# Kernel tuning notes

Hardware: AMD Instinct MI355X
Metric: run time of the kernel (lower is better)

Reference implementation:

```python
import jax, jax.numpy as jnp
import numpy as np

N_HEADS = 16
D_EMBD = 1024
D_HEAD = D_EMBD // N_HEADS
NEG_INF = -jnp.inf


def setup_inputs() -> dict:
    key = jax.random.key(0)
    k1, k2, k3, k4, k5 = jax.random.split(key, 5)
    b, s = 4, 2048
    scale_in = 1.0 / np.sqrt(D_EMBD)
    return {
        "x": jax.random.normal(k1, (b, s, D_EMBD), dtype=jnp.float32),
        "W_in": jax.random.normal(k2, (D_EMBD, 3 * D_EMBD), dtype=jnp.float32) * scale_in,
        "b_in": jax.random.normal(k3, (3 * D_EMBD,), dtype=jnp.float32) * 0.01,
        "W_out": jax.random.normal(k4, (D_EMBD, D_EMBD), dtype=jnp.float32) * scale_in,
        "b_out": jax.random.normal(k5, (D_EMBD,), dtype=jnp.float32) * 0.01,
    }


def reference(x, W_in, b_in, W_out, b_out):
    b, s, d = x.shape
    qkv = x @ W_in + b_in                      # [b, s, 3d]
    q, k, v = jnp.split(qkv, 3, axis=-1)
    # [b, s, d] -> [b, h, s, dh]
    def heads(t):
        return t.reshape(b, s, N_HEADS, D_HEAD).transpose(0, 2, 1, 3)
    q, k, v = heads(q), heads(k), heads(v)
    scores = jnp.einsum("bhqd,bhkd->bhqk", q, k)  # [b, h, s, s]
    # causal mask: mask strictly-upper triangle (future positions) with -inf,
    # applied before the sqrt(d_head) scale as in the original (equivalent math)
    mask = jnp.triu(jnp.ones((s, s), dtype=bool), k=1)
    scores = jnp.where(mask, NEG_INF, scores)
    scores = scores / jnp.sqrt(jnp.float32(D_HEAD)).astype(scores.dtype)
    attn = jax.nn.softmax(scores, axis=-1)
    out = jnp.einsum("bhqk,bhkd->bhqd", attn, v)   # [b, h, s, dh]
    out = out.transpose(0, 2, 1, 3).reshape(b, s, d)
    return out @ W_out + b_out
```

## Files before the change

### kernel.cpp

```cpp
#include <hip/hip_runtime.h>
#include <stdint.h>

#define AS1 __attribute__((address_space(1)))
#define AS3 __attribute__((address_space(3)))

typedef __bf16 bf16x8 __attribute__((ext_vector_type(8)));
typedef float f32x4 __attribute__((ext_vector_type(4)));
typedef unsigned short u16;
typedef unsigned int u32;

#define LOG2E 1.4426950408889634f

__device__ __forceinline__ u16 f2b(float f) {
    u32 u = __builtin_bit_cast(u32, f);
    u = (u + 0x7fffu + ((u >> 16) & 1u)) >> 16;
    return (u16)u;
}

__device__ __forceinline__ void gld16(const u16* g, u16* l) {
    __builtin_amdgcn_global_load_lds((const AS1 void*)g, (AS3 void*)l, 16, 0, 0);
}

__global__ void k_cvt(const float* __restrict__ in, u16* __restrict__ out, int n4) {
    int i = blockIdx.x * 256 + threadIdx.x;
    if (i >= n4) return;
    float4 v = reinterpret_cast<const float4*>(in)[i];
    ushort4 o;
    o.x = f2b(v.x); o.y = f2b(v.y); o.z = f2b(v.z); o.w = f2b(v.w);
    reinterpret_cast<ushort4*>(out)[i] = o;
}

__global__ void k_tr(const float* __restrict__ in, u16* __restrict__ out, int R, int C) {
    __shared__ float tl[64][65];
    int c0 = blockIdx.x * 64, r0 = blockIdx.y * 64;
    int tx = threadIdx.x & 63, ty = threadIdx.x >> 6;
#pragma unroll
    for (int i = 0; i < 16; ++i) {
        int r = i * 4 + ty;
        tl[r][tx] = in[(size_t)(r0 + r) * C + c0 + tx];
    }
    __syncthreads();
#pragma unroll
    for (int i = 0; i < 16; ++i) {
        int c = i * 4 + ty;
        out[(size_t)(c0 + c) * R + r0 + tx] = f2b(tl[tx][c]);
    }
}

template <int EPI>
__global__ __launch_bounds__(256, 2)
void k_gemm(const u16* __restrict__ A, const u16* __restrict__ BT,
            const float* __restrict__ bias,
            u16* __restrict__ qk, u16* __restrict__ vT,
            float* __restrict__ outf, int M, int N, int K) {
    __shared__ u16 sA[128 * 64];
    __shared__ u16 sB[128 * 64];
    const int t = threadIdx.x;
    const int lane = t & 63;
    const int w = t >> 6;
    const int lo = lane & 15, hi = lane >> 4;
    const int wr = w >> 1, wc = w & 1;
    const int m0 = blockIdx.x * 128, n0 = blockIdx.y * 128;

    const int srow = lane >> 3;
    const int scol = ((lane & 7) ^ srow) * 8;
    const int chunk0 = w * 4;

    f32x4 acc[4][4];
#pragma unroll
    for (int i = 0; i < 4; ++i)
#pragma unroll
        for (int j = 0; j < 4; ++j) acc[i][j] = f32x4{0.f, 0.f, 0.f, 0.f};

    char* sAc = (char*)sA;
    char* sBc = (char*)sB;

    for (int kt = 0; kt < K; kt += 64) {
        const u16* Ab = A + (size_t)m0 * K + kt;
        const u16* Bb = BT + (size_t)n0 * K + kt;
#pragma unroll
        for (int c = 0; c < 4; ++c) {
            int chunk = chunk0 + c;
            int row = chunk * 8 + srow;
            gld16(Ab + (size_t)row * K + scol, (u16*)(sAc + chunk * 1024));
            gld16(Bb + (size_t)row * K + scol, (u16*)(sBc + chunk * 1024));
        }
        __syncthreads();
#pragma unroll
        for (int ks = 0; ks < 2; ++ks) {
            bf16x8 af[4], bfr[4];
#pragma unroll
            for (int mf = 0; mf < 4; ++mf) {
                int row = wr * 64 + mf * 16 + lo;
                int byte = row * 128 + (((ks * 32 + hi * 8) * 2) ^ ((row & 7) << 4));
                af[mf] = *(const bf16x8*)(sAc + byte);
            }
#pragma unroll
            for (int nf = 0; nf < 4; ++nf) {
                int row = wc * 64 + nf * 16 + lo;
                int byte = row * 128 + (((ks * 32 + hi * 8) * 2) ^ ((row & 7) << 4));
                bfr[nf] = *(const bf16x8*)(sBc + byte);
            }
#pragma unroll
            for (int mf = 0; mf < 4; ++mf)
#pragma unroll
                for (int nf = 0; nf < 4; ++nf)
                    acc[mf][nf] = __builtin_amdgcn_mfma_f32_16x16x32_bf16(
                        af[mf], bfr[nf], acc[mf][nf], 0, 0, 0);
        }
        __syncthreads();
    }

    if (EPI == 0) {
#pragma unroll
        for (int nf = 0; nf < 4; ++nf) {
            int col = n0 + wc * 64 + nf * 16 + lo;
            float bv = bias[col];
#pragma unroll
            for (int mf = 0; mf < 4; ++mf) {
                int rowb = m0 + wr * 64 + mf * 16 + hi * 4;
                if (col < 2048) {
#pragma unroll
                    for (int r = 0; r < 4; ++r)
                        qk[(size_t)(rowb + r) * 2048 + col] = f2b(acc[mf][nf][r] + bv);
                } else {
                    int hd = col - 2048;
                    int hh = hd >> 6, dh = hd & 63;
                    int bb = rowb >> 11, s = rowb & 2047;
                    size_t base = ((size_t)(bb * 16 + hh) * 64 + dh) * 2048 + s;
#pragma unroll
                    for (int r = 0; r < 4; ++r)
                        vT[base + r] = f2b(acc[mf][nf][r] + bv);
                }
            }
        }
    } else {
#pragma unroll
        for (int nf = 0; nf < 4; ++nf) {
            int col = n0 + wc * 64 + nf * 16 + lo;
            float bv = bias[col];
#pragma unroll
            for (int mf = 0; mf < 4; ++mf) {
                int rowb = m0 + wr * 64 + mf * 16 + hi * 4;
#pragma unroll
                for (int r = 0; r < 4; ++r)
                    outf[(size_t)(rowb + r) * (size_t)N + col] = acc[mf][nf][r] + bv;
            }
        }
    }
}

__global__ __launch_bounds__(64, 4)
void k_attn(const u16* __restrict__ qk, const u16* __restrict__ vT,
            u16* __restrict__ attnout) {
    __shared__ u16 p_lds[16 * 128];
    const int lane = threadIdx.x & 63;
    const int lo = lane & 15, hi = lane >> 4;
    const int orig = blockIdx.x;
    const int wgid = (orig & 7) * 512 + (orig >> 3);
    const int j0 = wgid & 63;
    const int bh = wgid >> 6;
    const int h = bh & 15, b = bh >> 4;
    const int bS = b * 2048;
    const u16* vb = vT + (size_t)bh * (64 * 2048);
    const u16* kb = qk + (size_t)bS * 2048 + 1024 + h * 64;
    char* pb = (char*)p_lds;
    const float C1 = 0.125f * LOG2E;
    const int rsw = (lo & 7) << 4;

#pragma unroll 1
    for (int task = 0; task < 2; ++task) {
        const int j = task ? (127 - j0) : j0;
        const int qr0 = j * 16;
        const int qtile = j >> 3;
        const int qrow = qr0 + lo;

        bf16x8 qf[2];
#pragma unroll
        for (int ks = 0; ks < 2; ++ks)
            qf[ks] = *(const bf16x8*)(qk + (size_t)(bS + qrow) * 2048 + h * 64 +
                                      ks * 32 + hi * 8);

        f32x4 o[4];
#pragma unroll
        for (int n2 = 0; n2 < 4; ++n2) o[n2] = f32x4{0.f, 0.f, 0.f, 0.f};
        float rm = -1e30f, rl = 0.f;

        for (int kt = 0; kt <= qtile; ++kt) {
            f32x4 sc[8];
#pragma unroll
            for (int n = 0; n < 8; ++n) sc[n] = f32x4{0.f, 0.f, 0.f, 0.f};
            __builtin_amdgcn_s_setprio(1);
#pragma unroll
            for (int n = 0; n < 8; ++n) {
                const u16* kr = kb + (size_t)(kt * 128 + n * 16 + lo) * 2048;
                bf16x8 k0 = *(const bf16x8*)(kr + hi * 8);
                bf16x8 k1 = *(const bf16x8*)(kr + 32 + hi * 8);
                sc[n] = __builtin_amdgcn_mfma_f32_16x16x32_bf16(k0, qf[0], sc[n], 0, 0, 0);
                sc[n] = __builtin_amdgcn_mfma_f32_16x16x32_bf16(k1, qf[1], sc[n], 0, 0, 0);
            }
            __builtin_amdgcn_s_setprio(0);
            float pm = -1e30f;
            const int kb0 = kt * 128 + hi * 4;
#pragma unroll
            for (int n = 0; n < 8; ++n) {
#pragma unroll
                for (int r = 0; r < 4; ++r) {
                    float v = sc[n][r] * C1;
                    if (kb0 + n * 16 + r > qrow) v = -1e30f;
                    sc[n][r] = v;
                    pm = fmaxf(pm, v);
                }
            }
            pm = fmaxf(pm, __shfl_xor(pm, 16, 64));
            pm = fmaxf(pm, __shfl_xor(pm, 32, 64));
            float nm = fmaxf(rm, pm);
            float f = exp2f(rm - nm);
            rm = nm;
            float s = 0.f;
#pragma unroll
            for (int n = 0; n < 8; ++n)
#pragma unroll
                for (int r = 0; r < 4; ++r) {
                    float p = exp2f(sc[n][r] - nm);
                    sc[n][r] = p;
                    s += p;
                }
            s += __shfl_xor(s, 16, 64);
            s += __shfl_xor(s, 32, 64);
            rl = rl * f + s;
#pragma unroll
            for (int n2 = 0; n2 < 4; ++n2)
#pragma unroll
                for (int r = 0; r < 4; ++r) o[n2][r] *= f;
#pragma unroll
            for (int n = 0; n < 8; ++n) {
                u32 w0, w1;
                asm("v_cvt_pk_bf16_f32 %0, %1, %2" : "=v"(w0) : "v"(sc[n][0]), "v"(sc[n][1]));
                asm("v_cvt_pk_bf16_f32 %0, %1, %2" : "=v"(w1) : "v"(sc[n][2]), "v"(sc[n][3]));
                uint2 pkv; pkv.x = w0; pkv.y = w1;
                *(uint2*)(pb + lo * 256 + ((n * 32 + hi * 8) ^ rsw)) = pkv;
            }
            __builtin_amdgcn_s_setprio(1);
#pragma unroll
            for (int ks = 0; ks < 4; ++ks) {
                bf16x8 pa = *(const bf16x8*)(pb + lo * 256 + ((ks * 64 + hi * 16) ^ rsw));
#pragma unroll
                for (int n2 = 0; n2 < 4; ++n2) {
                    bf16x8 vf = *(const bf16x8*)(vb + (size_t)(n2 * 16 + lo) * 2048 +
                                                 kt * 128 + ks * 32 + hi * 8);
                    o[n2] = __builtin_amdgcn_mfma_f32_16x16x32_bf16(vf, pa, o[n2], 0, 0, 0);
                }
            }
            __builtin_amdgcn_s_setprio(0);
        }
        float inv = 1.0f / rl;
#pragma unroll
        for (int n2 = 0; n2 < 4; ++n2) {
            ushort4 st;
            st.x = f2b(o[n2][0] * inv);
            st.y = f2b(o[n2][1] * inv);
            st.z = f2b(o[n2][2] * inv);
            st.w = f2b(o[n2][3] * inv);
            *(ushort4*)(attnout + (size_t)(bS + qrow) * 1024 + h * 64 + n2 * 16 + hi * 4) = st;
        }
    }
}

extern "C" void kernel_launch(void* const* d_in, const int* in_sizes, int n_in,
                              void* d_out, int out_size, void* d_ws, size_t ws_size,
                              hipStream_t stream) {
    const float* x     = (const float*)d_in[0];
    const float* W_in  = (const float*)d_in[1];
    const float* b_in  = (const float*)d_in[2];
    const float* W_out = (const float*)d_in[3];
    const float* b_out = (const float*)d_in[4];
    float* out = (float*)d_out;

    char* ws = (char*)d_ws;
    u16* xb    = (u16*)(ws);
    u16* winT  = (u16*)(ws + 16777216);
    u16* woutT = (u16*)(ws + 23068672);
    u16* qkb   = (u16*)(ws + 25165824);
    u16* vTb   = (u16*)(ws + 58720256);
    u16* attno = (u16*)(ws + 75497472);

    k_cvt<<<8192, 256, 0, stream>>>(x, xb, 2097152);
    k_tr<<<dim3(48, 16), 256, 0, stream>>>(W_in, winT, 1024, 3072);
    k_tr<<<dim3(16, 16), 256, 0, stream>>>(W_out, woutT, 1024, 1024);
    k_gemm<0><<<dim3(64, 24), 256, 0, stream>>>(xb, winT, b_in, qkb, vTb, nullptr,
                                                8192, 3072, 1024);
    k_attn<<<4096, 64, 0, stream>>>(qkb, vTb, attno);
    k_gemm<1><<<dim3(64, 8), 256, 0, stream>>>(attno, woutT, b_out, nullptr, nullptr, out,
                                               8192, 1024, 1024);
}
```

Measured before the change: 423.7 us.

## Split attention into one tile per block and skip redundant rescales

Each attention workgroup now handles a single 16-row query tile instead of a paired light/heavy pair. The grid doubles to 8192 blocks, ordered heaviest-first, and launch bounds are raised to allow 8 waves per SIMD. The causal mask is applied only on the diagonal key tile. The online-softmax rescale is skipped when no lane's max increases, and the row-sum cross-lane reduction is deferred to the end. This cuts per-iteration VALU and shuffle work and should improve load balance, but loses the pairing's balanced per-block work and may pressure registers under the tighter occupancy bound.

```diff
diff --git a/kernel.cpp b/kernel.cpp
--- a/kernel.cpp
+++ b/kernel.cpp
@@ -150,16 +150,16 @@
     }
 }
 
-__global__ __launch_bounds__(64, 4)
+__global__ __launch_bounds__(64, 8)
 void k_attn(const u16* __restrict__ qk, const u16* __restrict__ vT,
             u16* __restrict__ attnout) {
     __shared__ u16 p_lds[16 * 128];
     const int lane = threadIdx.x & 63;
     const int lo = lane & 15, hi = lane >> 4;
     const int orig = blockIdx.x;
-    const int wgid = (orig & 7) * 512 + (orig >> 3);
-    const int j0 = wgid & 63;
-    const int bh = wgid >> 6;
+    const int wgid = (orig & 7) * 1024 + (orig >> 3);
+    const int bh = wgid >> 7;
+    const int j = 127 - (wgid & 127);
     const int h = bh & 15, b = bh >> 4;
     const int bS = b * 2048;
     const u16* vb = vT + (size_t)bh * (64 * 2048);
@@ -168,42 +168,40 @@
     const float C1 = 0.125f * LOG2E;
     const int rsw = (lo & 7) << 4;
 
-#pragma unroll 1
-    for (int task = 0; task < 2; ++task) {
-        const int j = task ? (127 - j0) : j0;
-        const int qr0 = j * 16;
-        const int qtile = j >> 3;
-        const int qrow = qr0 + lo;
-
-        bf16x8 qf[2];
-#pragma unroll
-        for (int ks = 0; ks < 2; ++ks)
-            qf[ks] = *(const bf16x8*)(qk + (size_t)(bS + qrow) * 2048 + h * 64 +
-                                      ks * 32 + hi * 8);
-
-        f32x4 o[4];
-#pragma unroll
-        for (int n2 = 0; n2 < 4; ++n2) o[n2] = f32x4{0.f, 0.f, 0.f, 0.f};
-        float rm = -1e30f, rl = 0.f;
-
-        for (int kt = 0; kt <= qtile; ++kt) {
-            f32x4 sc[8];
-#pragma unroll
-            for (int n = 0; n < 8; ++n) sc[n] = f32x4{0.f, 0.f, 0.f, 0.f};
-            __builtin_amdgcn_s_setprio(1);
-#pragma unroll
-            for (int n = 0; n < 8; ++n) {
-                const u16* kr = kb + (size_t)(kt * 128 + n * 16 + lo) * 2048;
-                bf16x8 k0 = *(const bf16x8*)(kr + hi * 8);
-                bf16x8 k1 = *(const bf16x8*)(kr + 32 + hi * 8);
-                sc[n] = __builtin_amdgcn_mfma_f32_16x16x32_bf16(k0, qf[0], sc[n], 0, 0, 0);
-                sc[n] = __builtin_amdgcn_mfma_f32_16x16x32_bf16(k1, qf[1], sc[n], 0, 0, 0);
-            }
-            __builtin_amdgcn_s_setprio(0);
-            float pm = -1e30f;
+    const int qtile = j >> 3;
+    const int qrow = j * 16 + lo;
+
+    bf16x8 qf[2];
+#pragma unroll
+    for (int ks = 0; ks < 2; ++ks)
+        qf[ks] = *(const bf16x8*)(qk + (size_t)(bS + qrow) * 2048 + h * 64 +
+                                  ks * 32 + hi * 8);
+
+    f32x4 o[4];
+#pragma unroll
+    for (int n2 = 0; n2 < 4; ++n2) o[n2] = f32x4{0.f, 0.f, 0.f, 0.f};
+    float rm = -1e30f;
+    float rl = 0.f;
+
+    for (int kt = 0; kt <= qtile; ++kt) {
+        f32x4 sc[8];
+#pragma unroll
+        for (int n = 0; n < 8; ++n) sc[n] = f32x4{0.f, 0.f, 0.f, 0.f};
+        __builtin_amdgcn_s_setprio(1);
+#pragma unroll
+        for (int n = 0; n < 8; ++n) {
+            const u16* kr = kb + (size_t)(kt * 128 + n * 16 + lo) * 2048;
+            bf16x8 k0 = *(const bf16x8*)(kr + hi * 8);
+            bf16x8 k1 = *(const bf16x8*)(kr + 32 + hi * 8);
+            sc[n] = __builtin_amdgcn_mfma_f32_16x16x32_bf16(k0, qf[0], sc[n], 0, 0, 0);
+            sc[n] = __builtin_amdgcn_mfma_f32_16x16x32_bf16(k1, qf[1], sc[n], 0, 0, 0);
+        }
+        __builtin_amdgcn_s_setprio(0);
+        float pm = -1e30f;
+        if (kt == qtile) {
             const int kb0 = kt * 128 + hi * 4;
 #pragma unroll
-            for (int n = 0; n < 8; ++n) {
+            for (int n = 0; n < 8; ++n)
 #pragma unroll
                 for (int r = 0; r < 4; ++r) {
                     float v = sc[n][r] * C1;
@@ -211,59 +209,70 @@
                     sc[n][r] = v;
                     pm = fmaxf(pm, v);
                 }
-            }
+        } else {
+#pragma unroll
+            for (int n = 0; n < 8; ++n)
+#pragma unroll
+                for (int r = 0; r < 4; ++r) {
+                    float v = sc[n][r] * C1;
+                    sc[n][r] = v;
+                    pm = fmaxf(pm, v);
+                }
+        }
+        if (!__all(pm <= rm)) {
             pm = fmaxf(pm, __shfl_xor(pm, 16, 64));
             pm = fmaxf(pm, __shfl_xor(pm, 32, 64));
             float nm = fmaxf(rm, pm);
             float f = exp2f(rm - nm);
             rm = nm;
-            float s = 0.f;
-#pragma unroll
-            for (int n = 0; n < 8; ++n)
-#pragma unroll
-                for (int r = 0; r < 4; ++r) {
-                    float p = exp2f(sc[n][r] - nm);
-                    sc[n][r] = p;
-                    s += p;
-                }
-            s += __shfl_xor(s, 16, 64);
-            s += __shfl_xor(s, 32, 64);
-            rl = rl * f + s;
+            rl *= f;
 #pragma unroll
             for (int n2 = 0; n2 < 4; ++n2)
 #pragma unroll
                 for (int r = 0; r < 4; ++r) o[n2][r] *= f;
-#pragma unroll
-            for (int n = 0; n < 8; ++n) {
-                u32 w0, w1;
-                asm("v_cvt_pk_bf16_f32 %0, %1, %2" : "=v"(w0) : "v"(sc[n][0]), "v"(sc[n][1]));
-                asm("v_cvt_pk_bf16_f32 %0, %1, %2" : "=v"(w1) : "v"(sc[n][2]), "v"(sc[n][3]));
-                uint2 pkv; pkv.x = w0; pkv.y = w1;
-                *(uint2*)(pb + lo * 256 + ((n * 32 + hi * 8) ^ rsw)) = pkv;
-            }
-            __builtin_amdgcn_s_setprio(1);
-#pragma unroll
-            for (int ks = 0; ks < 4; ++ks) {
-                bf16x8 pa = *(const bf16x8*)(pb + lo * 256 + ((ks * 64 + hi * 16) ^ rsw));
-#pragma unroll
-                for (int n2 = 0; n2 < 4; ++n2) {
-                    bf16x8 vf = *(const bf16x8*)(vb + (size_t)(n2 * 16 + lo) * 2048 +
-                                                 kt * 128 + ks * 32 + hi * 8);
-                    o[n2] = __builtin_amdgcn_mfma_f32_16x16x32_bf16(vf, pa, o[n2], 0, 0, 0);
-                }
-            }
-            __builtin_amdgcn_s_setprio(0);
-        }
-        float inv = 1.0f / rl;
-#pragma unroll
-        for (int n2 = 0; n2 < 4; ++n2) {
-            ushort4 st;
-            st.x = f2b(o[n2][0] * inv);
-            st.y = f2b(o[n2][1] * inv);
-            st.z = f2b(o[n2][2] * inv);
-            st.w = f2b(o[n2][3] * inv);
-            *(ushort4*)(attnout + (size_t)(bS + qrow) * 1024 + h * 64 + n2 * 16 + hi * 4) = st;
-        }
+        }
+        float s = 0.f;
+#pragma unroll
+        for (int n = 0; n < 8; ++n)
+#pragma unroll
+            for (int r = 0; r < 4; ++r) {
+                float p = exp2f(sc[n][r] - rm);
+                sc[n][r] = p;
+                s += p;
+            }
+        rl += s;
+#pragma unroll
+        for (int n = 0; n < 8; ++n) {
+            u32 w0, w1;
+            asm("v_cvt_pk_bf16_f32 %0, %1, %2" : "=v"(w0) : "v"(sc[n][0]), "v"(sc[n][1]));
+            asm("v_cvt_pk_bf16_f32 %0, %1, %2" : "=v"(w1) : "v"(sc[n][2]), "v"(sc[n][3]));
+            uint2 pkv; pkv.x = w0; pkv.y = w1;
+            *(uint2*)(pb + lo * 256 + ((n * 32 + hi * 8) ^ rsw)) = pkv;
+        }
+        __builtin_amdgcn_s_setprio(1);
+#pragma unroll
+        for (int ks = 0; ks < 4; ++ks) {
+            bf16x8 pa = *(const bf16x8*)(pb + lo * 256 + ((ks * 64 + hi * 16) ^ rsw));
+#pragma unroll
+            for (int n2 = 0; n2 < 4; ++n2) {
+                bf16x8 vf = *(const bf16x8*)(vb + (size_t)(n2 * 16 + lo) * 2048 +
+                                             kt * 128 + ks * 32 + hi * 8);
+                o[n2] = __builtin_amdgcn_mfma_f32_16x16x32_bf16(vf, pa, o[n2], 0, 0, 0);
+            }
+        }
+        __builtin_amdgcn_s_setprio(0);
+    }
+    rl += __shfl_xor(rl, 16, 64);
+    rl += __shfl_xor(rl, 32, 64);
+    float inv = 1.0f / rl;
+#pragma unroll
+    for (int n2 = 0; n2 < 4; ++n2) {
+        ushort4 st;
+        st.x = f2b(o[n2][0] * inv);
+        st.y = f2b(o[n2][1] * inv);
+        st.z = f2b(o[n2][2] * inv);
+        st.w = f2b(o[n2][3] * inv);
+        *(ushort4*)(attnout + (size_t)(bS + qrow) * 1024 + h * 64 + n2 * 16 + hi * 4) = st;
     }
 }
 
@@ -290,7 +299,7 @@
     k_tr<<<dim3(16, 16), 256, 0, stream>>>(W_out, woutT, 1024, 1024);
     k_gemm<0><<<dim3(64, 24), 256, 0, stream>>>(xb, winT, b_in, qkb, vTb, nullptr,
                                                 8192, 3072, 1024);
-    k_attn<<<4096, 64, 0, stream>>>(qkb, vTb, attno);
+    k_attn<<<8192, 64, 0, stream>>>(qkb, vTb, attno);
     k_gemm<1><<<dim3(64, 8), 256, 0, stream>>>(attno, woutT, b_out, nullptr, nullptr, out,
                                                8192, 1024, 1024);
 }
```

Result: slower. 634.0 us (+49.6%).
